# Performance work log

Hardware: AMD Instinct MI355X
Metric: run time of the kernel (lower is better)

## Reference

```python
import jax, jax.numpy as jnp
import numpy as np

B, S, SE, D, V, L, H = 32, 256, 1024, 512, 8000, 4, 8
EPS = 1e-3   # keras BatchNormalization default epsilon
NEG = -1e9


def _heads(x, W, b):
    Bx, Sx, Dx = x.shape
    return (jnp.einsum('bsd,de->bse', x, W) + b).reshape(Bx, Sx, H, Dx // H).transpose(0, 2, 1, 3)


def mha(q_in, kv_in, Wq, bq, Wk, bk, Wv, bv, Wo, bo, causal):
    dk = q_in.shape[-1] // H
    q = _heads(q_in, Wq, bq)   # [B,H,Sq,dk]
    k = _heads(kv_in, Wk, bk)  # [B,H,Sk,dk]
    v = _heads(kv_in, Wv, bv)
    scores = jnp.einsum('bhqd,bhkd->bhqk', q, k) / jnp.sqrt(jnp.asarray(dk, q.dtype))
    if causal:
        # original loop uses values = x[:, :j, :] -> token j attends to STRICTLY previous tokens;
        # token 0 has zero keys, so its attention output is exactly zero (before Wo bias).
        Sq, Sk = scores.shape[-2], scores.shape[-1]
        mask = jnp.arange(Sk)[None, :] < jnp.arange(Sq)[:, None]
        attn = jax.nn.softmax(jnp.where(mask, scores, NEG), axis=-1)
        attn = jnp.where(mask, attn, 0.0)
    else:
        attn = jax.nn.softmax(scores, axis=-1)
    out = jnp.einsum('bhqk,bhkd->bhqd', attn, v)
    out = out.transpose(0, 2, 1, 3).reshape(q_in.shape[0], q_in.shape[1], -1)
    return out @ Wo + bo


def bn(x, gamma, beta, mean, var):
    # keras BatchNorm, inference mode, axis=-1
    return gamma * (x - mean) * jax.lax.rsqrt(var + EPS) + beta


def setup_inputs():
    key = jax.random.key(0)
    ks = iter(jax.random.split(key, 80))

    def rn(*shape):
        return jax.random.normal(next(ks), shape, jnp.float32) * 0.02

    inp = {
        'sequence': jax.random.randint(next(ks), (B, S), 0, V, jnp.int32),
        'encoder_output': jax.random.normal(next(ks), (B, SE, D), jnp.float32),
        'pos_encodings': jax.random.normal(next(ks), (S, D), jnp.float32),
        'emb': rn(V, D),
        'Wout': rn(D, V), 'bout': jnp.zeros((V,), jnp.float32),
        'W1': rn(L, D, 512), 'b1': jnp.zeros((L, 512), jnp.float32),
        'W2': rn(L, 512, D), 'b2': jnp.zeros((L, D), jnp.float32),
    }
    for p in ('bot', 'mid'):
        for nm in ('Wq', 'Wk', 'Wv', 'Wo'):
            inp[f'{nm}_{p}'] = rn(L, D, D)
        for nm in ('bq', 'bk', 'bv', 'bo'):
            inp[f'{nm}_{p}'] = jnp.zeros((L, D), jnp.float32)
    for p in ('bot', 'mid', 'ffn'):
        inp[f'gamma_{p}'] = jnp.ones((L, D), jnp.float32)
        inp[f'beta_{p}'] = jnp.zeros((L, D), jnp.float32)
        inp[f'mean_{p}'] = jnp.zeros((L, D), jnp.float32)
        inp[f'var_{p}'] = jnp.ones((L, D), jnp.float32)
    return inp


def reference(sequence, encoder_output, pos_encodings, emb, Wout, bout, W1, b1, W2, b2,
              Wq_bot, Wk_bot, Wv_bot, Wo_bot, bq_bot, bk_bot, bv_bot, bo_bot,
              Wq_mid, Wk_mid, Wv_mid, Wo_mid, bq_mid, bk_mid, bv_mid, bo_mid,
              gamma_bot, beta_bot, mean_bot, var_bot,
              gamma_mid, beta_mid, mean_mid, var_mid,
              gamma_ffn, beta_ffn, mean_ffn, var_ffn):
    x = emb[sequence] + pos_encodings[None, :, :]  # [B,S,D]
    for i in range(L):
        a = mha(x, x, Wq_bot[i], bq_bot[i], Wk_bot[i], bk_bot[i], Wv_bot[i], bv_bot[i], Wo_bot[i], bo_bot[i], True)
        x = bn(x + a, gamma_bot[i], beta_bot[i], mean_bot[i], var_bot[i])
        a = mha(x, encoder_output, Wq_mid[i], bq_mid[i], Wk_mid[i], bk_mid[i], Wv_mid[i], bv_mid[i], Wo_mid[i], bo_mid[i], False)
        x = bn(x + a, gamma_mid[i], beta_mid[i], mean_mid[i], var_mid[i])
        f = jax.nn.relu(x @ W1[i] + b1[i]) @ W2[i] + b2[i]
        x = bn(x + f, gamma_ffn[i], beta_ffn[i], mean_ffn[i], var_ffn[i])
    return x @ Wout + bout  # logits [B,S,V]
```

## Files before the change

kernel.cpp:

```cpp
#include <hip/hip_runtime.h>
#include <hip/hip_fp16.h>

typedef unsigned short u16;
typedef _Float16 half8 __attribute__((ext_vector_type(8)));
typedef _Float16 half4 __attribute__((ext_vector_type(4)));
typedef float floatx4 __attribute__((ext_vector_type(4)));

#define NB 32
#define NS 256
#define NSE 1024
#define ND 512
#define NV 8000
#define NL 4
#define NH 8
#define NDK 64
#define BN_EPS 1e-3f

typedef const __attribute__((address_space(1))) void* gas_ptr;
typedef __attribute__((address_space(3))) void* las_ptr;
__device__ __forceinline__ void gload16(const void* g, void* l) {
    __builtin_amdgcn_global_load_lds((gas_ptr)g, (las_ptr)l, 16, 0, 0);
}

__global__ __launch_bounds__(256) void k_cast(const float* __restrict__ in, _Float16* __restrict__ out) {
    size_t i = ((size_t)blockIdx.x * 256 + threadIdx.x) * 8;
    float4 a = *(const float4*)(in + i);
    float4 b = *(const float4*)(in + i + 4);
    half8 o;
    o[0] = (_Float16)a.x; o[1] = (_Float16)a.y; o[2] = (_Float16)a.z; o[3] = (_Float16)a.w;
    o[4] = (_Float16)b.x; o[5] = (_Float16)b.y; o[6] = (_Float16)b.z; o[7] = (_Float16)b.w;
    *(half8*)(out + i) = o;
}

__global__ __launch_bounds__(256) void k_embed(const int* __restrict__ seq,
                                               const float* __restrict__ emb,
                                               const float* __restrict__ pos,
                                               _Float16* __restrict__ x) {
    size_t i = ((size_t)blockIdx.x * 256 + threadIdx.x) * 8;
    int tok = (int)(i / ND);
    int d = (int)(i % ND);
    int s = tok % NS;
    int t = seq[tok];
    const float* ep = emb + (size_t)t * ND + d;
    const float* pp = pos + (size_t)s * ND + d;
    half8 o;
    for (int j = 0; j < 8; j++) o[j] = (_Float16)(ep[j] + pp[j]);
    *(half8*)(x + i) = o;
}

__global__ __launch_bounds__(256) void k_bnres(const _Float16* __restrict__ xin, const _Float16* __restrict__ a,
                                               const float* __restrict__ gamma, const float* __restrict__ beta,
                                               const float* __restrict__ mean, const float* __restrict__ var,
                                               _Float16* __restrict__ xout) {
    size_t i = ((size_t)blockIdx.x * 256 + threadIdx.x) * 8;
    int d = (int)(i % ND);
    half8 xv = *(const half8*)(xin + i);
    half8 av = *(const half8*)(a + i);
    half8 o;
    for (int j = 0; j < 8; j++) {
        float v = (float)xv[j] + (float)av[j];
        float r = rsqrtf(var[d + j] + BN_EPS);
        o[j] = (_Float16)(((v - mean[d + j]) * r) * gamma[d + j] + beta[d + j]);
    }
    *(half8*)(xout + i) = o;
}

__global__ void k_transpose_w(const float* __restrict__ in, _Float16* __restrict__ out, int R, int C) {
    __shared__ float tile[32][33];
    int b = blockIdx.z;
    int c0 = blockIdx.x * 32, r0 = blockIdx.y * 32;
    const float* pin = in + (size_t)b * R * C;
    _Float16* pout = out + (size_t)b * R * C;
    int tx = threadIdx.x, ty = threadIdx.y;
    for (int j = 0; j < 32; j += 8)
        tile[ty + j][tx] = pin[(size_t)(r0 + ty + j) * C + c0 + tx];
    __syncthreads();
    for (int j = 0; j < 32; j += 8)
        pout[(size_t)(c0 + ty + j) * R + r0 + tx] = (_Float16)tile[tx][ty + j];
}

template<int BM>
__global__ __launch_bounds__(256) void k_gemm(const _Float16* __restrict__ A, const _Float16* __restrict__ Bt,
                                              const float* __restrict__ bias, void* __restrict__ Cout,
                                              int M, int N, int K, int relu, int outmode, int Sb) {
    constexpr int BN = 128;
    constexpr int BK = 64;
    constexpr int MI = BM / 32;
    __shared__ __align__(16) _Float16 smem[BM * BK + BN * BK];
    _Float16* As = smem;
    _Float16* Bs = smem + BM * BK;

    int tid = threadIdx.x;
    int wid = tid >> 6, lane = tid & 63, quad = lane >> 4, r = lane & 15;

    int nwg = gridDim.x * gridDim.y;
    int orig = blockIdx.y * gridDim.x + blockIdx.x;
    int q8 = nwg >> 3, r8 = nwg & 7;
    int xcd = orig & 7, loc = orig >> 3;
    int swz = (xcd < r8 ? xcd * (q8 + 1) : r8 * (q8 + 1) + (xcd - r8) * q8) + loc;
    int m0 = (swz / gridDim.x) * BM;
    int n0 = (swz % gridDim.x) * BN;

    int wm = (wid >> 1) * (BM / 2);
    int wn = (wid & 1) * 64;

    floatx4 zf = {0.f, 0.f, 0.f, 0.f};
    floatx4 acc[MI][4];
    for (int i = 0; i < MI; i++) for (int j = 0; j < 4; j++) acc[i][j] = zf;

    int srow = wid * 8 + (lane >> 3);
    int scol = (lane & 7) * 8;

    for (int k0 = 0; k0 < K; k0 += BK) {
        __syncthreads();
        {
            const _Float16* abase = A + (size_t)(m0 + srow) * K + k0 + scol;
            for (int i = 0; i < BM / 32; i++)
                gload16(abase + (size_t)i * 32 * K, As + (i * 32 + wid * 8) * BK);
            const _Float16* bbase = Bt + (size_t)(n0 + srow) * K + k0 + scol;
            for (int i = 0; i < 4; i++)
                gload16(bbase + (size_t)i * 32 * K, Bs + (i * 32 + wid * 8) * BK);
        }
        __syncthreads();
        for (int ks = 0; ks < BK; ks += 32) {
            half8 af[MI], bg[4];
#pragma unroll
            for (int i = 0; i < MI; i++) af[i] = *(const half8*)&As[(wm + i * 16 + r) * BK + ks + quad * 8];
#pragma unroll
            for (int j = 0; j < 4; j++)  bg[j] = *(const half8*)&Bs[(wn + j * 16 + r) * BK + ks + quad * 8];
#pragma unroll
            for (int i = 0; i < MI; i++)
#pragma unroll
                for (int j = 0; j < 4; j++)
                    acc[i][j] = __builtin_amdgcn_mfma_f32_16x16x32_f16(af[i], bg[j], acc[i][j], 0, 0, 0);
        }
    }

    __syncthreads();

    if (outmode == 1) {
        for (int i = 0; i < MI; i++) {
            int grow = m0 + wm + i * 16 + quad * 4;
            int b = grow / Sb, s = grow - b * Sb;
            _Float16* outp = (_Float16*)Cout + (size_t)b * N * Sb + s;
#pragma unroll
            for (int j = 0; j < 4; j++) {
                int col = n0 + wn + j * 16 + r;
                float bv = bias[col];
                half4 h;
#pragma unroll
                for (int g = 0; g < 4; g++) {
                    float v = acc[i][j][g] + bv;
                    if (relu) v = fmaxf(v, 0.0f);
                    h[g] = (_Float16)v;
                }
                *(half4*)(outp + (size_t)col * Sb) = h;
            }
        }
    } else {
        float* Ep = (float*)(void*)smem + wid * (16 * 68);
        int rr = lane >> 4;
        int c = (lane & 15) * 4;
        for (int i = 0; i < MI; i++) {
#pragma unroll
            for (int j = 0; j < 4; j++) {
                int col = n0 + wn + j * 16 + r;
                float bv = (col < N) ? bias[col] : 0.0f;
#pragma unroll
                for (int g = 0; g < 4; g++) {
                    float v = acc[i][j][g] + bv;
                    if (relu) v = fmaxf(v, 0.0f);
                    Ep[(quad * 4 + g) * 68 + j * 16 + r] = v;
                }
            }
            if (outmode == 0) {
#pragma unroll
                for (int p = 0; p < 4; p++) {
                    float4 v = *(float4*)&Ep[(p * 4 + rr) * 68 + c];
                    half4 h;
                    h[0] = (_Float16)v.x; h[1] = (_Float16)v.y; h[2] = (_Float16)v.z; h[3] = (_Float16)v.w;
                    int grow = m0 + wm + i * 16 + p * 4 + rr;
                    *(half4*)&((_Float16*)Cout)[(size_t)grow * N + n0 + wn + c] = h;
                }
            } else {
#pragma unroll
                for (int p = 0; p < 4; p++) {
                    int gcol = n0 + wn + c;
                    if (gcol < N) {
                        float4 v = *(float4*)&Ep[(p * 4 + rr) * 68 + c];
                        int grow = m0 + wm + i * 16 + p * 4 + rr;
                        *(float4*)&((float*)Cout)[(size_t)grow * N + gcol] = v;
                    }
                }
            }
        }
    }
}

__global__ __launch_bounds__(256) void k_attn(const _Float16* __restrict__ Q, const _Float16* __restrict__ Kb,
                                              const _Float16* __restrict__ Vt, _Float16* __restrict__ O,
                                              int Sk, int causal) {
    __shared__ _Float16 Plds[4][16][72];
    int qt = blockIdx.x, h = blockIdx.y, b = blockIdx.z;
    int tid = threadIdx.x;
    int w = tid >> 6, lane = tid & 63, quad = lane >> 4, r = lane & 15;
    int qbase = qt * 64 + w * 16;

    floatx4 zf = {0.f, 0.f, 0.f, 0.f};
    half8 aq[2];
    const _Float16* qptr = Q + (size_t)(b * NS + qbase + r) * ND + h * NDK;
    aq[0] = *(const half8*)(qptr + quad * 8);
    aq[1] = *(const half8*)(qptr + 32 + quad * 8);

    floatx4 Of[4];
    for (int j = 0; j < 4; j++) Of[j] = zf;
    float mrow[4], lrow[4];
    for (int g = 0; g < 4; g++) { mrow[g] = -1e30f; lrow[g] = 0.0f; }

    int ntiles = causal ? (qt + 1) : (Sk >> 6);

    for (int kt = 0; kt < ntiles; kt++) {
        floatx4 sc[4];
        for (int j = 0; j < 4; j++) sc[j] = zf;
        for (int t = 0; t < 2; t++) {
            for (int j = 0; j < 4; j++) {
                const _Float16* kptr = Kb + (size_t)(b * Sk + kt * 64 + j * 16 + r) * ND + h * NDK + t * 32 + quad * 8;
                half8 bk = *(const half8*)kptr;
                sc[j] = __builtin_amdgcn_mfma_f32_16x16x32_f16(aq[t], bk, sc[j], 0, 0, 0);
            }
        }
        float s[4][4], tmax[4];
        for (int g = 0; g < 4; g++) tmax[g] = -1e30f;
        for (int j = 0; j < 4; j++) {
            int key = kt * 64 + j * 16 + r;
            for (int g = 0; g < 4; g++) {
                float v = sc[j][g] * 0.125f;
                int qi = qbase + quad * 4 + g;
                if (causal && key >= qi) v = -1e30f;
                s[j][g] = v;
                tmax[g] = fmaxf(tmax[g], v);
            }
        }
        for (int off = 1; off < 16; off <<= 1)
            for (int g = 0; g < 4; g++)
                tmax[g] = fmaxf(tmax[g], __shfl_xor(tmax[g], off, 64));
        float alpha[4], psum[4];
        for (int g = 0; g < 4; g++) {
            float mnew = fmaxf(mrow[g], tmax[g]);
            alpha[g] = (mnew <= -1e29f) ? 1.0f : __expf(mrow[g] - mnew);
            mrow[g] = mnew;
            psum[g] = 0.0f;
        }
        for (int j = 0; j < 4; j++) {
            for (int g = 0; g < 4; g++) {
                float p = (s[j][g] <= -1e29f) ? 0.0f : __expf(s[j][g] - mrow[g]);
                psum[g] += p;
                Plds[w][quad * 4 + g][j * 16 + r] = (_Float16)p;
            }
        }
        for (int off = 1; off < 16; off <<= 1)
            for (int g = 0; g < 4; g++)
                psum[g] += __shfl_xor(psum[g], off, 64);
        for (int g = 0; g < 4; g++) lrow[g] = lrow[g] * alpha[g] + psum[g];
        for (int j = 0; j < 4; j++)
            for (int g = 0; g < 4; g++)
                Of[j][g] *= alpha[g];
        __syncthreads();
        for (int t = 0; t < 2; t++) {
            half8 ap = *(const half8*)&Plds[w][r][t * 32 + quad * 8];
            for (int j = 0; j < 4; j++) {
                const _Float16* vptr = Vt + (size_t)((b * NH + h) * NDK + j * 16 + r) * Sk + kt * 64 + t * 32 + quad * 8;
                half8 bv = *(const half8*)vptr;
                Of[j] = __builtin_amdgcn_mfma_f32_16x16x32_f16(ap, bv, Of[j], 0, 0, 0);
            }
        }
        __syncthreads();
    }
    for (int j = 0; j < 4; j++) {
        for (int g = 0; g < 4; g++) {
            int row = qbase + quad * 4 + g;
            float inv = (lrow[g] > 0.f) ? 1.0f / lrow[g] : 0.0f;
            O[(size_t)(b * NS + row) * ND + h * NDK + j * 16 + r] = (_Float16)(Of[j][g] * inv);
        }
    }
}

extern "C" void kernel_launch(void* const* d_in, const int* in_sizes, int n_in,
                              void* d_out, int out_size, void* d_ws, size_t ws_size,
                              hipStream_t stream) {
    const int*   seq  = (const int*)d_in[0];
    const float* enc  = (const float*)d_in[1];
    const float* pos  = (const float*)d_in[2];
    const float* emb  = (const float*)d_in[3];
    const float* Wout = (const float*)d_in[4];
    const float* bout = (const float*)d_in[5];
    const float* W1   = (const float*)d_in[6];
    const float* b1   = (const float*)d_in[7];
    const float* W2   = (const float*)d_in[8];
    const float* b2   = (const float*)d_in[9];
    const float* Wq_bot = (const float*)d_in[10];
    const float* Wk_bot = (const float*)d_in[11];
    const float* Wv_bot = (const float*)d_in[12];
    const float* Wo_bot = (const float*)d_in[13];
    const float* bq_bot = (const float*)d_in[14];
    const float* bk_bot = (const float*)d_in[15];
    const float* bv_bot = (const float*)d_in[16];
    const float* bo_bot = (const float*)d_in[17];
    const float* Wq_mid = (const float*)d_in[18];
    const float* Wk_mid = (const float*)d_in[19];
    const float* Wv_mid = (const float*)d_in[20];
    const float* Wo_mid = (const float*)d_in[21];
    const float* bq_mid = (const float*)d_in[22];
    const float* bk_mid = (const float*)d_in[23];
    const float* bv_mid = (const float*)d_in[24];
    const float* bo_mid = (const float*)d_in[25];
    const float* gam[3] = {(const float*)d_in[26], (const float*)d_in[30], (const float*)d_in[34]};
    const float* bet[3] = {(const float*)d_in[27], (const float*)d_in[31], (const float*)d_in[35]};
    const float* mea[3] = {(const float*)d_in[28], (const float*)d_in[32], (const float*)d_in[36]};
    const float* vr [3] = {(const float*)d_in[29], (const float*)d_in[33], (const float*)d_in[37]};

    char* wp = (char*)d_ws;
    auto alloc = [&](size_t elems) -> _Float16* {
        _Float16* p = (_Float16*)wp;
        wp += ((elems * 2 + 255) / 256) * 256;
        return p;
    };
    const size_t DD = (size_t)ND * ND;
    const int NVP = 8064;
    _Float16* WqTb = alloc(NL * DD);
    _Float16* WkTb = alloc(NL * DD);
    _Float16* WvTb = alloc(NL * DD);
    _Float16* WoTb = alloc(NL * DD);
    _Float16* WqTm = alloc(NL * DD);
    _Float16* WkTm = alloc(NL * DD);
    _Float16* WvTm = alloc(NL * DD);
    _Float16* WoTm = alloc(NL * DD);
    _Float16* W1T  = alloc(NL * DD);
    _Float16* W2T  = alloc(NL * DD);
    _Float16* WoutT = alloc((size_t)NVP * ND);
    const size_t XSZ = (size_t)NB * NS * ND;
    _Float16* x   = alloc(XSZ);
    _Float16* qb  = alloc(XSZ);
    _Float16* kb  = alloc(XSZ);
    _Float16* vts = alloc(XSZ);
    _Float16* ao  = alloc(XSZ);
    const size_t ESZ = (size_t)NB * NSE * ND;
    _Float16* ench  = alloc(ESZ);
    _Float16* kenc  = alloc(ESZ);
    _Float16* vtenc = alloc(ESZ);

    hipMemsetAsync(WoutT + (size_t)NV * ND, 0, (size_t)(NVP - NV) * ND * sizeof(_Float16), stream);

    dim3 tb(32, 8);
    k_transpose_w<<<dim3(ND / 32, ND / 32, NL), tb, 0, stream>>>(Wq_bot, WqTb, ND, ND);
    k_transpose_w<<<dim3(ND / 32, ND / 32, NL), tb, 0, stream>>>(Wk_bot, WkTb, ND, ND);
    k_transpose_w<<<dim3(ND / 32, ND / 32, NL), tb, 0, stream>>>(Wv_bot, WvTb, ND, ND);
    k_transpose_w<<<dim3(ND / 32, ND / 32, NL), tb, 0, stream>>>(Wo_bot, WoTb, ND, ND);
    k_transpose_w<<<dim3(ND / 32, ND / 32, NL), tb, 0, stream>>>(Wq_mid, WqTm, ND, ND);
    k_transpose_w<<<dim3(ND / 32, ND / 32, NL), tb, 0, stream>>>(Wk_mid, WkTm, ND, ND);
    k_transpose_w<<<dim3(ND / 32, ND / 32, NL), tb, 0, stream>>>(Wv_mid, WvTm, ND, ND);
    k_transpose_w<<<dim3(ND / 32, ND / 32, NL), tb, 0, stream>>>(Wo_mid, WoTm, ND, ND);
    k_transpose_w<<<dim3(ND / 32, ND / 32, NL), tb, 0, stream>>>(W1, W1T, ND, ND);
    k_transpose_w<<<dim3(ND / 32, ND / 32, NL), tb, 0, stream>>>(W2, W2T, ND, ND);
    k_transpose_w<<<dim3(NV / 32, ND / 32, 1), tb, 0, stream>>>(Wout, WoutT, ND, NV);
    k_cast<<<dim3((int)(ESZ / 8 / 256)), 256, 0, stream>>>(enc, ench);

    auto gemm = [&](const _Float16* A, const _Float16* Bt, const float* bias, void* C,
                    int M, int N, int relu, int outmode, int Sb, int bm) {
        if (bm == 64)
            k_gemm<64><<<dim3((N + 127) / 128, M / 64), 256, 0, stream>>>(A, Bt, bias, C, M, N, ND, relu, outmode, Sb);
        else
            k_gemm<128><<<dim3((N + 127) / 128, M / 128), 256, 0, stream>>>(A, Bt, bias, C, M, N, ND, relu, outmode, Sb);
    };

    k_embed<<<dim3((int)(XSZ / 8 / 256)), 256, 0, stream>>>(seq, emb, pos, x);

    const int M = NB * NS;
    const int ME = NB * NSE;
    for (int l = 0; l < NL; l++) {
        size_t wofs = (size_t)l * DD;
        size_t bofs = (size_t)l * ND;
        gemm(x, WqTb + wofs, bq_bot + bofs, qb, M, ND, 0, 0, 0, 64);
        gemm(x, WkTb + wofs, bk_bot + bofs, kb, M, ND, 0, 0, 0, 64);
        gemm(x, WvTb + wofs, bv_bot + bofs, vts, M, ND, 0, 1, NS, 64);
        k_attn<<<dim3(NS / 64, NH, NB), 256, 0, stream>>>(qb, kb, vts, ao, NS, 1);
        gemm(ao, WoTb + wofs, bo_bot + bofs, kb, M, ND, 0, 0, 0, 64);
        k_bnres<<<dim3((int)(XSZ / 8 / 256)), 256, 0, stream>>>(x, kb, gam[0] + bofs, bet[0] + bofs, mea[0] + bofs, vr[0] + bofs, x);
        gemm(x, WqTm + wofs, bq_mid + bofs, qb, M, ND, 0, 0, 0, 64);
        gemm(ench, WkTm + wofs, bk_mid + bofs, kenc, ME, ND, 0, 0, 0, 128);
        gemm(ench, WvTm + wofs, bv_mid + bofs, vtenc, ME, ND, 0, 1, NSE, 128);
        k_attn<<<dim3(NS / 64, NH, NB), 256, 0, stream>>>(qb, kenc, vtenc, ao, NSE, 0);
        gemm(ao, WoTm + wofs, bo_mid + bofs, kb, M, ND, 0, 0, 0, 64);
        k_bnres<<<dim3((int)(XSZ / 8 / 256)), 256, 0, stream>>>(x, kb, gam[1] + bofs, bet[1] + bofs, mea[1] + bofs, vr[1] + bofs, x);
        gemm(x, W1T + wofs, b1 + bofs, qb, M, ND, 1, 0, 0, 64);
        gemm(qb, W2T + wofs, b2 + bofs, kb, M, ND, 0, 0, 0, 64);
        k_bnres<<<dim3((int)(XSZ / 8 / 256)), 256, 0, stream>>>(x, kb, gam[2] + bofs, bet[2] + bofs, mea[2] + bofs, vr[2] + bofs, x);
    }
    gemm(x, WoutT, bout, (float*)d_out, M, NV, 0, 2, 0, 128);
}
```

Measured before the change: 2.041 ms.

## Fuse QKV and encoder KV projections and fold BatchNorm-residual into GEMM epilogue

The bottom-attention Q, K and V weights are concatenated so one GEMM with N=1536 writes all three outputs, with the segment selecting the per-output layout. The cross-attention encoder K and V projections are merged the same way. The separate residual+BatchNorm kernel is removed: the Wo and W2 GEMMs now add the residual, apply the BN affine transform in the epilogue and write x in place. The 64-row GEMMs also switch to a BK of 128. Together these cut kernel launches and the round trips of intermediate activations through memory, at the cost of a heavier, branchier epilogue and higher LDS use per block.

```diff
diff --git a/kernel.cpp b/kernel.cpp
--- a/kernel.cpp
+++ b/kernel.cpp
@@ -1,7 +1,6 @@
 #include <hip/hip_runtime.h>
 #include <hip/hip_fp16.h>
 
-typedef unsigned short u16;
 typedef _Float16 half8 __attribute__((ext_vector_type(8)));
 typedef _Float16 half4 __attribute__((ext_vector_type(4)));
 typedef float floatx4 __attribute__((ext_vector_type(4)));
@@ -11,6 +10,7 @@
 #define NSE 1024
 #define ND 512
 #define NV 8000
+#define NVP 8064
 #define NL 4
 #define NH 8
 #define NDK 64
@@ -48,29 +48,13 @@
     *(half8*)(x + i) = o;
 }
 
-__global__ __launch_bounds__(256) void k_bnres(const _Float16* __restrict__ xin, const _Float16* __restrict__ a,
-                                               const float* __restrict__ gamma, const float* __restrict__ beta,
-                                               const float* __restrict__ mean, const float* __restrict__ var,
-                                               _Float16* __restrict__ xout) {
-    size_t i = ((size_t)blockIdx.x * 256 + threadIdx.x) * 8;
-    int d = (int)(i % ND);
-    half8 xv = *(const half8*)(xin + i);
-    half8 av = *(const half8*)(a + i);
-    half8 o;
-    for (int j = 0; j < 8; j++) {
-        float v = (float)xv[j] + (float)av[j];
-        float r = rsqrtf(var[d + j] + BN_EPS);
-        o[j] = (_Float16)(((v - mean[d + j]) * r) * gamma[d + j] + beta[d + j]);
-    }
-    *(half8*)(xout + i) = o;
-}
-
-__global__ void k_transpose_w(const float* __restrict__ in, _Float16* __restrict__ out, int R, int C) {
+__global__ void k_transpose_w(const float* __restrict__ in, _Float16* __restrict__ out, int R, int C,
+                              long long ostride) {
     __shared__ float tile[32][33];
     int b = blockIdx.z;
     int c0 = blockIdx.x * 32, r0 = blockIdx.y * 32;
     const float* pin = in + (size_t)b * R * C;
-    _Float16* pout = out + (size_t)b * R * C;
+    _Float16* pout = out + (size_t)b * ostride;
     int tx = threadIdx.x, ty = threadIdx.y;
     for (int j = 0; j < 32; j += 8)
         tile[ty + j][tx] = pin[(size_t)(r0 + ty + j) * C + c0 + tx];
@@ -79,14 +63,21 @@
         pout[(size_t)(c0 + ty + j) * R + r0 + tx] = (_Float16)tile[tx][ty + j];
 }
 
-template<int BM>
-__global__ __launch_bounds__(256) void k_gemm(const _Float16* __restrict__ A, const _Float16* __restrict__ Bt,
-                                              const float* __restrict__ bias, void* __restrict__ Cout,
-                                              int M, int N, int K, int relu, int outmode, int Sb) {
+template<int BM, int BK>
+__global__ __launch_bounds__(256) void k_gemm(
+    const _Float16* __restrict__ A, const _Float16* __restrict__ Bt,
+    const float* __restrict__ bias0, const float* __restrict__ bias1, const float* __restrict__ bias2,
+    void* __restrict__ C0, void* __restrict__ C1, void* __restrict__ C2,
+    int M, int N, int K, int relu, int mode, int Sb,
+    const _Float16* __restrict__ xres,
+    const float* __restrict__ bng, const float* __restrict__ bnb,
+    const float* __restrict__ bnm, const float* __restrict__ bnv) {
     constexpr int BN = 128;
-    constexpr int BK = 64;
     constexpr int MI = BM / 32;
-    __shared__ __align__(16) _Float16 smem[BM * BK + BN * BK];
+    constexpr int TPR = BK / 8;
+    constexpr int RPW = 64 / TPR;
+    constexpr int RPI = 4 * RPW;
+    __shared__ __align__(16) _Float16 smem[(BM + BN) * BK];
     _Float16* As = smem;
     _Float16* Bs = smem + BM * BK;
 
@@ -108,20 +99,25 @@
     floatx4 acc[MI][4];
     for (int i = 0; i < MI; i++) for (int j = 0; j < 4; j++) acc[i][j] = zf;
 
-    int srow = wid * 8 + (lane >> 3);
-    int scol = (lane & 7) * 8;
+    int srow = wid * RPW + lane / TPR;
+    int scol = (lane % TPR) * 8;
 
     for (int k0 = 0; k0 < K; k0 += BK) {
         __syncthreads();
         {
             const _Float16* abase = A + (size_t)(m0 + srow) * K + k0 + scol;
-            for (int i = 0; i < BM / 32; i++)
-                gload16(abase + (size_t)i * 32 * K, As + (i * 32 + wid * 8) * BK);
+            _Float16* asl = As + (size_t)(wid * RPW) * BK;
+#pragma unroll
+            for (int i = 0; i < BM / RPI; i++)
+                gload16(abase + (size_t)(i * RPI) * K, asl + (size_t)(i * RPI) * BK);
             const _Float16* bbase = Bt + (size_t)(n0 + srow) * K + k0 + scol;
-            for (int i = 0; i < 4; i++)
-                gload16(bbase + (size_t)i * 32 * K, Bs + (i * 32 + wid * 8) * BK);
+            _Float16* bsl = Bs + (size_t)(wid * RPW) * BK;
+#pragma unroll
+            for (int i = 0; i < BN / RPI; i++)
+                gload16(bbase + (size_t)(i * RPI) * K, bsl + (size_t)(i * RPI) * BK);
         }
         __syncthreads();
+#pragma unroll
         for (int ks = 0; ks < BK; ks += 32) {
             half8 af[MI], bg[4];
 #pragma unroll
@@ -138,23 +134,34 @@
 
     __syncthreads();
 
-    if (outmode == 1) {
+    int seg = 0, nloc = n0, om = mode;
+    const float* bias = bias0;
+    char* C = (char*)C0;
+    if (mode == 4) {
+        seg = n0 >> 9; nloc = n0 & 511;
+        om = (seg == 2) ? 1 : 0;
+        C = (char*)(seg == 0 ? C0 : (seg == 1 ? C1 : C2));
+        bias = (seg == 0) ? bias0 : ((seg == 1) ? bias1 : bias2);
+    } else if (mode == 5) {
+        seg = n0 >> 9; nloc = n0 & 511;
+        om = seg ? 1 : 0;
+        C = (char*)(seg ? C1 : C0);
+        bias = seg ? bias1 : bias0;
+    }
+
+    if (om == 1) {
         for (int i = 0; i < MI; i++) {
             int grow = m0 + wm + i * 16 + quad * 4;
             int b = grow / Sb, s = grow - b * Sb;
-            _Float16* outp = (_Float16*)Cout + (size_t)b * N * Sb + s;
+            _Float16* outp = (_Float16*)C + (size_t)b * 512 * Sb + s;
 #pragma unroll
             for (int j = 0; j < 4; j++) {
-                int col = n0 + wn + j * 16 + r;
-                float bv = bias[col];
+                int cb = nloc + wn + j * 16 + r;
+                float bv = bias[cb];
                 half4 h;
 #pragma unroll
-                for (int g = 0; g < 4; g++) {
-                    float v = acc[i][j][g] + bv;
-                    if (relu) v = fmaxf(v, 0.0f);
-                    h[g] = (_Float16)v;
-                }
-                *(half4*)(outp + (size_t)col * Sb) = h;
+                for (int g = 0; g < 4; g++) h[g] = (_Float16)(acc[i][j][g] + bv);
+                *(half4*)(outp + (size_t)cb * Sb) = h;
             }
         }
     } else {
@@ -164,8 +171,8 @@
         for (int i = 0; i < MI; i++) {
 #pragma unroll
             for (int j = 0; j < 4; j++) {
-                int col = n0 + wn + j * 16 + r;
-                float bv = (col < N) ? bias[col] : 0.0f;
+                int cb = nloc + wn + j * 16 + r;
+                float bv = (om == 2) ? (cb < N ? bias[cb] : 0.0f) : bias[cb];
 #pragma unroll
                 for (int g = 0; g < 4; g++) {
                     float v = acc[i][j][g] + bv;
@@ -173,23 +180,43 @@
                     Ep[(quad * 4 + g) * 68 + j * 16 + r] = v;
                 }
             }
-            if (outmode == 0) {
+            int grow0 = m0 + wm + i * 16;
+            int cb = nloc + wn + c;
+            if (om == 0) {
 #pragma unroll
                 for (int p = 0; p < 4; p++) {
                     float4 v = *(float4*)&Ep[(p * 4 + rr) * 68 + c];
                     half4 h;
                     h[0] = (_Float16)v.x; h[1] = (_Float16)v.y; h[2] = (_Float16)v.z; h[3] = (_Float16)v.w;
-                    int grow = m0 + wm + i * 16 + p * 4 + rr;
-                    *(half4*)&((_Float16*)Cout)[(size_t)grow * N + n0 + wn + c] = h;
+                    *(half4*)&((_Float16*)C)[(size_t)(grow0 + p * 4 + rr) * 512 + cb] = h;
+                }
+            } else if (om == 3) {
+                float4 g4 = *(const float4*)(bng + cb);
+                float4 b4 = *(const float4*)(bnb + cb);
+                float4 m4 = *(const float4*)(bnm + cb);
+                float4 v4 = *(const float4*)(bnv + cb);
+                float s0 = g4.x * rsqrtf(v4.x + BN_EPS);
+                float s1 = g4.y * rsqrtf(v4.y + BN_EPS);
+                float s2 = g4.z * rsqrtf(v4.z + BN_EPS);
+                float s3 = g4.w * rsqrtf(v4.w + BN_EPS);
+#pragma unroll
+                for (int p = 0; p < 4; p++) {
+                    int grow = grow0 + p * 4 + rr;
+                    float4 v = *(float4*)&Ep[(p * 4 + rr) * 68 + c];
+                    half4 xv = *(const half4*)(xres + (size_t)grow * 512 + cb);
+                    half4 h;
+                    h[0] = (_Float16)((v.x + (float)xv[0] - m4.x) * s0 + b4.x);
+                    h[1] = (_Float16)((v.y + (float)xv[1] - m4.y) * s1 + b4.y);
+                    h[2] = (_Float16)((v.z + (float)xv[2] - m4.z) * s2 + b4.z);
+                    h[3] = (_Float16)((v.w + (float)xv[3] - m4.w) * s3 + b4.w);
+                    *(half4*)&((_Float16*)C)[(size_t)grow * 512 + cb] = h;
                 }
             } else {
-#pragma unroll
-                for (int p = 0; p < 4; p++) {
-                    int gcol = n0 + wn + c;
-                    if (gcol < N) {
+                if (cb < N) {
+#pragma unroll
+                    for (int p = 0; p < 4; p++) {
                         float4 v = *(float4*)&Ep[(p * 4 + rr) * 68 + c];
-                        int grow = m0 + wm + i * 16 + p * 4 + rr;
-                        *(float4*)&((float*)Cout)[(size_t)grow * N + gcol] = v;
+                        *(float4*)&((float*)C)[(size_t)(grow0 + p * 4 + rr) * N + cb] = v;
                     }
                 }
             }
@@ -326,18 +353,14 @@
         return p;
     };
     const size_t DD = (size_t)ND * ND;
-    const int NVP = 8064;
-    _Float16* WqTb = alloc(NL * DD);
-    _Float16* WkTb = alloc(NL * DD);
-    _Float16* WvTb = alloc(NL * DD);
-    _Float16* WoTb = alloc(NL * DD);
-    _Float16* WqTm = alloc(NL * DD);
-    _Float16* WkTm = alloc(NL * DD);
-    _Float16* WvTm = alloc(NL * DD);
-    _Float16* WoTm = alloc(NL * DD);
-    _Float16* W1T  = alloc(NL * DD);
-    _Float16* W2T  = alloc(NL * DD);
-    _Float16* WoutT = alloc((size_t)NVP * ND);
+    _Float16* WqkvTb = alloc(NL * 3 * DD);
+    _Float16* WoTb   = alloc(NL * DD);
+    _Float16* WqTm   = alloc(NL * DD);
+    _Float16* WkvTm  = alloc(NL * 2 * DD);
+    _Float16* WoTm   = alloc(NL * DD);
+    _Float16* W1T    = alloc(NL * DD);
+    _Float16* W2T    = alloc(NL * DD);
+    _Float16* WoutT  = alloc((size_t)NVP * ND);
     const size_t XSZ = (size_t)NB * NS * ND;
     _Float16* x   = alloc(XSZ);
     _Float16* qb  = alloc(XSZ);
@@ -352,49 +375,48 @@
     hipMemsetAsync(WoutT + (size_t)NV * ND, 0, (size_t)(NVP - NV) * ND * sizeof(_Float16), stream);
 
     dim3 tb(32, 8);
-    k_transpose_w<<<dim3(ND / 32, ND / 32, NL), tb, 0, stream>>>(Wq_bot, WqTb, ND, ND);
-    k_transpose_w<<<dim3(ND / 32, ND / 32, NL), tb, 0, stream>>>(Wk_bot, WkTb, ND, ND);
-    k_transpose_w<<<dim3(ND / 32, ND / 32, NL), tb, 0, stream>>>(Wv_bot, WvTb, ND, ND);
-    k_transpose_w<<<dim3(ND / 32, ND / 32, NL), tb, 0, stream>>>(Wo_bot, WoTb, ND, ND);
-    k_transpose_w<<<dim3(ND / 32, ND / 32, NL), tb, 0, stream>>>(Wq_mid, WqTm, ND, ND);
-    k_transpose_w<<<dim3(ND / 32, ND / 32, NL), tb, 0, stream>>>(Wk_mid, WkTm, ND, ND);
-    k_transpose_w<<<dim3(ND / 32, ND / 32, NL), tb, 0, stream>>>(Wv_mid, WvTm, ND, ND);
-    k_transpose_w<<<dim3(ND / 32, ND / 32, NL), tb, 0, stream>>>(Wo_mid, WoTm, ND, ND);
-    k_transpose_w<<<dim3(ND / 32, ND / 32, NL), tb, 0, stream>>>(W1, W1T, ND, ND);
-    k_transpose_w<<<dim3(ND / 32, ND / 32, NL), tb, 0, stream>>>(W2, W2T, ND, ND);
-    k_transpose_w<<<dim3(NV / 32, ND / 32, 1), tb, 0, stream>>>(Wout, WoutT, ND, NV);
+    const long long S1 = (long long)DD, S2 = (long long)(2 * DD), S3 = (long long)(3 * DD);
+    k_transpose_w<<<dim3(16, 16, NL), tb, 0, stream>>>(Wq_bot, WqkvTb,          ND, ND, S3);
+    k_transpose_w<<<dim3(16, 16, NL), tb, 0, stream>>>(Wk_bot, WqkvTb + DD,     ND, ND, S3);
+    k_transpose_w<<<dim3(16, 16, NL), tb, 0, stream>>>(Wv_bot, WqkvTb + 2 * DD, ND, ND, S3);
+    k_transpose_w<<<dim3(16, 16, NL), tb, 0, stream>>>(Wo_bot, WoTb,            ND, ND, S1);
+    k_transpose_w<<<dim3(16, 16, NL), tb, 0, stream>>>(Wq_mid, WqTm,            ND, ND, S1);
+    k_transpose_w<<<dim3(16, 16, NL), tb, 0, stream>>>(Wk_mid, WkvTm,           ND, ND, S2);
+    k_transpose_w<<<dim3(16, 16, NL), tb, 0, stream>>>(Wv_mid, WkvTm + DD,      ND, ND, S2);
+    k_transpose_w<<<dim3(16, 16, NL), tb, 0, stream>>>(Wo_mid, WoTm,            ND, ND, S1);
+    k_transpose_w<<<dim3(16, 16, NL), tb, 0, stream>>>(W1,     W1T,             ND, ND, S1);
+    k_transpose_w<<<dim3(16, 16, NL), tb, 0, stream>>>(W2,     W2T,             ND, ND, S1);
+    k_transpose_w<<<dim3(NV / 32, 16, 1), tb, 0, stream>>>(Wout, WoutT, ND, NV, S1);
     k_cast<<<dim3((int)(ESZ / 8 / 256)), 256, 0, stream>>>(enc, ench);
-
-    auto gemm = [&](const _Float16* A, const _Float16* Bt, const float* bias, void* C,
-                    int M, int N, int relu, int outmode, int Sb, int bm) {
-        if (bm == 64)
-            k_gemm<64><<<dim3((N + 127) / 128, M / 64), 256, 0, stream>>>(A, Bt, bias, C, M, N, ND, relu, outmode, Sb);
-        else
-            k_gemm<128><<<dim3((N + 127) / 128, M / 128), 256, 0, stream>>>(A, Bt, bias, C, M, N, ND, relu, outmode, Sb);
+    k_embed<<<dim3((int)(XSZ / 8 / 256)), 256, 0, stream>>>(seq, emb, pos, x);
+
+    auto gemm64 = [&](const _Float16* A, const _Float16* Bt, const float* b0, void* Cp,
+                      int relu, int mode, const _Float16* xr, const float* g, const float* be,
+                      const float* me, const float* ve) {
+        k_gemm<64, 128><<<dim3(4, 128), 256, 0, stream>>>(A, Bt, b0, nullptr, nullptr,
+            Cp, nullptr, nullptr, 8192, 512, 512, relu, mode, 0, xr, g, be, me, ve);
     };
 
-    k_embed<<<dim3((int)(XSZ / 8 / 256)), 256, 0, stream>>>(seq, emb, pos, x);
-
-    const int M = NB * NS;
-    const int ME = NB * NSE;
     for (int l = 0; l < NL; l++) {
         size_t wofs = (size_t)l * DD;
         size_t bofs = (size_t)l * ND;
-        gemm(x, WqTb + wofs, bq_bot + bofs, qb, M, ND, 0, 0, 0, 64);
-        gemm(x, WkTb + wofs, bk_bot + bofs, kb, M, ND, 0, 0, 0, 64);
-        gemm(x, WvTb + wofs, bv_bot + bofs, vts, M, ND, 0, 1, NS, 64);
+        k_gemm<128, 64><<<dim3(12, 64), 256, 0, stream>>>(x, WqkvTb + (size_t)l * 3 * DD,
+            bq_bot + bofs, bk_bot + bofs, bv_bot + bofs, qb, kb, vts,
+            8192, 1536, 512, 0, 4, NS, nullptr, nullptr, nullptr, nullptr, nullptr);
         k_attn<<<dim3(NS / 64, NH, NB), 256, 0, stream>>>(qb, kb, vts, ao, NS, 1);
-        gemm(ao, WoTb + wofs, bo_bot + bofs, kb, M, ND, 0, 0, 0, 64);
-        k_bnres<<<dim3((int)(XSZ / 8 / 256)), 256, 0, stream>>>(x, kb, gam[0] + bofs, bet[0] + bofs, mea[0] + bofs, vr[0] + bofs, x);
-        gemm(x, WqTm + wofs, bq_mid + bofs, qb, M, ND, 0, 0, 0, 64);
-        gemm(ench, WkTm + wofs, bk_mid + bofs, kenc, ME, ND, 0, 0, 0, 128);
-        gemm(ench, WvTm + wofs, bv_mid + bofs, vtenc, ME, ND, 0, 1, NSE, 128);
+        gemm64(ao, WoTb + wofs, bo_bot + bofs, x, 0, 3, x,
+               gam[0] + bofs, bet[0] + bofs, mea[0] + bofs, vr[0] + bofs);
+        gemm64(x, WqTm + wofs, bq_mid + bofs, qb, 0, 0, nullptr, nullptr, nullptr, nullptr, nullptr);
+        k_gemm<128, 64><<<dim3(8, 256), 256, 0, stream>>>(ench, WkvTm + (size_t)l * 2 * DD,
+            bk_mid + bofs, bv_mid + bofs, nullptr, kenc, vtenc, nullptr,
+            32768, 1024, 512, 0, 5, NSE, nullptr, nullptr, nullptr, nullptr, nullptr);
         k_attn<<<dim3(NS / 64, NH, NB), 256, 0, stream>>>(qb, kenc, vtenc, ao, NSE, 0);
-        gemm(ao, WoTm + wofs, bo_mid + bofs, kb, M, ND, 0, 0, 0, 64);
-        k_bnres<<<dim3((int)(XSZ / 8 / 256)), 256, 0, stream>>>(x, kb, gam[1] + bofs, bet[1] + bofs, mea[1] + bofs, vr[1] + bofs, x);
-        gemm(x, W1T + wofs, b1 + bofs, qb, M, ND, 1, 0, 0, 64);
-        gemm(qb, W2T + wofs, b2 + bofs, kb, M, ND, 0, 0, 0, 64);
-        k_bnres<<<dim3((int)(XSZ / 8 / 256)), 256, 0, stream>>>(x, kb, gam[2] + bofs, bet[2] + bofs, mea[2] + bofs, vr[2] + bofs, x);
-    }
-    gemm(x, WoutT, bout, (float*)d_out, M, NV, 0, 2, 0, 128);
-}
+        gemm64(ao, WoTm + wofs, bo_mid + bofs, x, 0, 3, x,
+               gam[1] + bofs, bet[1] + bofs, mea[1] + bofs, vr[1] + bofs);
+        gemm64(x, W1T + wofs, b1 + bofs, qb, 1, 0, nullptr, nullptr, nullptr, nullptr, nullptr);
+        gemm64(qb, W2T + wofs, b2 + bofs, x, 0, 3, x,
+               gam[2] + bofs, bet[2] + bofs, mea[2] + bofs, vr[2] + bofs);
+    }
+    k_gemm<128, 64><<<dim3(63, 64), 256, 0, stream>>>(x, WoutT, bout, nullptr, nullptr,
+        d_out, nullptr, nullptr, 8192, NV, 512, 0, 2, 0, nullptr, nullptr, nullptr, nullptr, nullptr);
+}
```

Measured after the change: 1.972 ms. -3.4%, faster.
